# Performance work log

Measured on AMD Instinct MI355X. Metric: run time of the kernel, lower is better.

The kernel has to match this reference:

```python
import jax, jax.numpy as jnp
import numpy as np

N_HEAD = 8  # config.n_head

def _ln(x, g, b):
    # eqx.nn.LayerNorm, eps=1e-5
    m = x.mean(-1, keepdims=True)
    v = ((x - m) ** 2).mean(-1, keepdims=True)
    return (x - m) / jnp.sqrt(v + 1e-5) * g + b

def _lin(x, w, b):
    # eqx.nn.Linear: weight [out, in]
    return x @ w.T + b

def _heads(t):
    B, T, C = t.shape
    return t.reshape(B, T, N_HEAD, C // N_HEAD).transpose(0, 2, 1, 3)  # [B,H,T,d]

def _merge(t):
    B, H, T, d = t.shape
    return t.transpose(0, 2, 1, 3).reshape(B, T, H * d)

def setup_inputs() -> dict:
    key = jax.random.key(0)
    B, T1, T2, C, INNER, NIN = 4, 4096, 4096, 512, 2048, 2
    ks = jax.random.split(key, 16)
    w = lambda k, *s: 0.02 * jax.random.normal(k, s, dtype=jnp.float32)
    return {
        'x': jax.random.normal(ks[0], (B, T1, C), dtype=jnp.float32),
        'ys': jax.random.normal(ks[1], (NIN, B, T2, C), dtype=jnp.float32),
        'ln1_g': jnp.ones((C,)), 'ln1_b': jnp.zeros((C,)),
        'ln2_g': jnp.ones((NIN, C)), 'ln2_b': jnp.zeros((NIN, C)),
        'ln3_g': jnp.ones((C,)), 'ln3_b': jnp.zeros((C,)),
        'ln4_g': jnp.ones((C,)), 'ln4_b': jnp.zeros((C,)),
        'ln5_g': jnp.ones((C,)), 'ln5_b': jnp.zeros((C,)),
        'ca_wq': w(ks[2], C, C), 'ca_bq': jnp.zeros((C,)),
        'ca_wk': w(ks[3], NIN, C, C), 'ca_bk': jnp.zeros((NIN, C)),
        'ca_wv': w(ks[4], NIN, C, C), 'ca_bv': jnp.zeros((NIN, C)),
        'ca_wo': w(ks[5], C, C), 'ca_bo': jnp.zeros((C,)),
        'sa_wq': w(ks[6], C, C), 'sa_bq': jnp.zeros((C,)),
        'sa_wk': w(ks[7], C, C), 'sa_bk': jnp.zeros((C,)),
        'sa_wv': w(ks[8], C, C), 'sa_bv': jnp.zeros((C,)),
        'sa_wo': w(ks[9], C, C), 'sa_bo': jnp.zeros((C,)),
        'ffn1_w1': w(ks[10], INNER, C), 'ffn1_b1': jnp.zeros((INNER,)),
        'ffn1_w2': w(ks[11], C, INNER), 'ffn1_b2': jnp.zeros((C,)),
        'ffn2_w1': w(ks[12], INNER, C), 'ffn2_b1': jnp.zeros((INNER,)),
        'ffn2_w2': w(ks[13], C, INNER), 'ffn2_b2': jnp.zeros((C,)),
    }

def reference(x, ys, ln1_g, ln1_b, ln2_g, ln2_b, ln3_g, ln3_b, ln4_g, ln4_b, ln5_g, ln5_b,
              ca_wq, ca_bq, ca_wk, ca_bk, ca_wv, ca_bv, ca_wo, ca_bo,
              sa_wq, sa_bq, sa_wk, sa_bk, sa_wv, sa_bv, sa_wo, sa_bo,
              ffn1_w1, ffn1_b1, ffn1_w2, ffn1_b2, ffn2_w1, ffn2_b1, ffn2_w2, ffn2_b2):
    n_inputs = ys.shape[0]
    # ---- linear cross attention ----
    xn = _ln(x, ln1_g, ln1_b)
    q = jax.nn.softmax(_heads(_lin(xn, ca_wq, ca_bq)), axis=-1)  # [B,H,T1,d]
    out = q
    for i in range(n_inputs):  # small fixed branch count
        yn = _ln(ys[i], ln2_g[i], ln2_b[i])
        k = jax.nn.softmax(_heads(_lin(yn, ca_wk[i], ca_bk[i])), axis=-1)  # [B,H,T2,d]
        v = _heads(_lin(yn, ca_wv[i], ca_bv[i]))
        k_sum = k.sum(axis=-2, keepdims=True)                       # [B,H,1,d]
        D_inv = 1.0 / ((q * k_sum).sum(axis=-1, keepdims=True) + 1e-8)
        ctx = jnp.einsum('bhnd,bhnv->bhdv', k, v)                   # [B,H,d,d]
        out = out + jnp.einsum('bhqd,bhdv->bhqv', q, ctx) * D_inv
    x = x + _lin(_merge(out), ca_wo, ca_bo)
    # ---- FFN 1 ----
    xn = _ln(x, ln3_g, ln3_b)
    x = x + _lin(jax.nn.gelu(_lin(xn, ffn1_w1, ffn1_b1)), ffn1_w2, ffn1_b2)
    # ---- linear self attention (attn_type='l1') ----
    xn = _ln(x, ln4_g, ln4_b)
    q = jax.nn.softmax(_heads(_lin(xn, sa_wq, sa_bq)), axis=-1)
    k = jax.nn.softmax(_heads(_lin(xn, sa_wk, sa_bk)), axis=-1)
    v = _heads(_lin(xn, sa_wv, sa_bv))
    k_sum = k.sum(axis=-2, keepdims=True)
    D_inv = 1.0 / (q * k_sum).sum(axis=-1, keepdims=True)  # no eps in 'l1' branch
    ctx = jnp.einsum('bhnd,bhnv->bhdv', k, v)
    sa = jnp.einsum('bhqd,bhdv->bhqv', q, ctx) * D_inv + q
    x = x + _lin(_merge(sa), sa_wo, sa_bo)
    # ---- FFN 2 ----
    xn = _ln(x, ln5_g, ln5_b)
    x = x + _lin(jax.nn.gelu(_lin(xn, ffn2_w1, ffn2_b1)), ffn2_w2, ffn2_b2)
    return x
```

## Files before the change

kernel.cpp:

```cpp
#include <hip/hip_runtime.h>
#include <hip/hip_bf16.h>
#include <math.h>
#include <stdint.h>

typedef unsigned short u16;
typedef __attribute__((ext_vector_type(8))) short bh8;
typedef __attribute__((ext_vector_type(4))) float fx4;

#define DEV static __device__ __forceinline__

DEV float bf2f(u16 u){ union{unsigned u; float f;} v; v.u = ((unsigned)u)<<16; return v.f; }
DEV u16 f2bf(float f){ union{float f; unsigned u;} v; v.f = f;
  return (u16)((v.u + 0x7fffu + ((v.u>>16)&1u))>>16); }

DEV void async16(const u16* g, u16* l){
  __builtin_amdgcn_global_load_lds((__attribute__((address_space(1))) void*)(uintptr_t)g,
                                   (__attribute__((address_space(3))) void*)l, 16, 0, 0);
}

DEV size_t faddr(int row, int col, int Kbuf){
  return (size_t)(row>>4)*((size_t)Kbuf*16)
       + (size_t)((col>>3)*128 + (row&15)*8 + (col&7));
}

DEV float gelu_fast(float x){
  float x2 = x*x;
  float t  = __builtin_fmaf(x2, -0.071354816f, -1.5957691216f);
  float e  = __expf(x*t);
  return __fdividef(x, 1.f + e);
}

DEV int2 xcd_swz(){
  const int gx  = gridDim.x;
  const int ord = blockIdx.y*gx + blockIdx.x;
  const int nwg = gx*gridDim.y;
  const int wg  = (ord&7)*(nwg>>3) + (ord>>3);
  int2 r; r.x = wg % gx; r.y = wg / gx; return r;
}

struct WDesc { const float* src[14]; int off[14]; };
__global__ __launch_bounds__(256) void convw_kernel(WDesc d, u16* __restrict__ dst){
  int i = blockIdx.x*256 + threadIdx.x;
  int s = 0;
  #pragma unroll
  for(int j=1;j<14;j++) if(i >= d.off[j]) s = j;
  dst[i] = f2bf(d.src[s][i - d.off[s]]);
}

DEV float wsum64(float s){
  s += __shfl_xor(s,1,64);  s += __shfl_xor(s,2,64);  s += __shfl_xor(s,4,64);
  s += __shfl_xor(s,8,64);  s += __shfl_xor(s,16,64); s += __shfl_xor(s,32,64);
  return s;
}
DEV void ln_row(const float* xrow, const float* g, const float* bta, u16* orow, int lane){
  const float4* xr = (const float4*)xrow + lane*2;
  float4 a = xr[0], c = xr[1];
  float s = a.x+a.y+a.z+a.w + c.x+c.y+c.z+c.w;
  float mean = wsum64(s) * (1.f/512.f);
  float d0=a.x-mean,d1=a.y-mean,d2=a.z-mean,d3=a.w-mean;
  float d4=c.x-mean,d5=c.y-mean,d6=c.z-mean,d7=c.w-mean;
  float sv = d0*d0+d1*d1+d2*d2+d3*d3+d4*d4+d5*d5+d6*d6+d7*d7;
  float rstd = rsqrtf(wsum64(sv)*(1.f/512.f) + 1e-5f);
  const float4* gr = (const float4*)g   + lane*2;
  const float4* br = (const float4*)bta + lane*2;
  float4 g0=gr[0], g1=gr[1], b0=br[0], b1=br[1];
  bh8 o;
  o[0]=(short)f2bf(d0*rstd*g0.x+b0.x); o[1]=(short)f2bf(d1*rstd*g0.y+b0.y);
  o[2]=(short)f2bf(d2*rstd*g0.z+b0.z); o[3]=(short)f2bf(d3*rstd*g0.w+b0.w);
  o[4]=(short)f2bf(d4*rstd*g1.x+b1.x); o[5]=(short)f2bf(d5*rstd*g1.y+b1.y);
  o[6]=(short)f2bf(d6*rstd*g1.z+b1.z); o[7]=(short)f2bf(d7*rstd*g1.w+b1.w);
  *(bh8*)(orow + (size_t)lane*128) = o;
}
__global__ __launch_bounds__(256) void ln_kernel(const float* __restrict__ x,
    const float* __restrict__ g, const float* __restrict__ bta, u16* __restrict__ out){
  int row  = blockIdx.x*4 + (threadIdx.x>>6);
  u16* orow = out + (size_t)(row>>4)*8192 + (size_t)(row&15)*8;
  ln_row(x + (size_t)row*512, g, bta, orow, threadIdx.x&63);
}
__global__ __launch_bounds__(256) void lny_kernel(const float* __restrict__ ys,
    const float* __restrict__ g2, const float* __restrict__ b2, u16* __restrict__ out){
  int row  = blockIdx.x*4 + (threadIdx.x>>6);
  int i = row>>14;
  u16* orow = out + (size_t)(row>>4)*8192 + (size_t)(row&15)*8;
  ln_row(ys + (size_t)row*512, g2 + i*512, b2 + i*512, orow, threadIdx.x&63);
}

#define BSTAGE128(Wb, K, kk, buf)                                                    \
    async16(Wb + (size_t)srow*(K)      + (kk) + scol, &lsB[buf][(w*32   )*32]);      \
    async16(Wb + (size_t)(srow+16)*(K) + (kk) + scol, &lsB[buf][(w*32+16)*32]);

#define APREF4(AF, K, kk)                                                            \
    _Pragma("unroll")                                                                \
    for(int t=0;t<4;t++)                                                             \
      AF[t] = *(const bh8*)(Alane + (size_t)t*16*(K) + (size_t)(kk)*16);

#define MFMA128(AF, CUR)                                                             \
    { bh8 bfx[4];                                                                    \
      _Pragma("unroll")                                                              \
      for(int t=0;t<4;t++)                                                           \
        bfx[t] = *(const bh8*)&lsB[CUR][(wn*64+t*16+l15)*32 + rsw*8];                \
      _Pragma("unroll")                                                              \
      for(int mt=0;mt<4;mt++)                                                        \
        _Pragma("unroll")                                                            \
        for(int nt=0;nt<4;nt++)                                                      \
          acc[mt][nt] = __builtin_amdgcn_mfma_f32_16x16x32_bf16(AF[mt], bfx[nt], acc[mt][nt], 0,0,0); }

#define CSTEP128(AFU, AFP, CUR, jj, Wb, K)                                           \
    if((jj)+1<NS){                                                                   \
      BSTAGE128(Wb, K, ((jj)+1)*32, (CUR)^1)                                         \
      asm volatile("" ::: "memory");                                                 \
      APREF4(AFP, K, ((jj)+1)*32)                                                    \
      asm volatile("s_waitcnt vmcnt(10)" ::: "memory");                              \
    } else {                                                                         \
      asm volatile("s_waitcnt vmcnt(0)" ::: "memory");                               \
    }                                                                                \
    __builtin_amdgcn_s_barrier();                                                    \
    MFMA128(AFU, CUR)                                                                \
    __builtin_amdgcn_s_barrier();

#define KLOOP_CNT128(Ab, Wb, K, WTILE)                                               \
  const int srow = w*32 + (lane>>2);                                                 \
  const int scol = (((lane&3) ^ ((srow>>1)&3)) * 8);                                 \
  const int rsw  = ((l15>>1)&3) ^ quad;                                              \
  const u16* Alane = (Ab) + (size_t)(WTILE)*16*(K) + lane*8;                         \
  bh8 afA[4], afB[4];                                                                \
  BSTAGE128(Wb, K, 0, 0)                                                             \
  asm volatile("" ::: "memory");                                                     \
  APREF4(afA, K, 0)                                                                  \
  const int NS = (K)>>5;                                                             \
  for(int j=0;j<NS;j+=2){                                                            \
    CSTEP128(afA, afB, 0, j,   Wb, K)                                                \
    CSTEP128(afB, afA, 1, j+1, Wb, K)                                                \
  }

#define SSTEP128(AFU, AFP, CUR, jj, Wb, K)                                           \
    if((jj)+1<NS){                                                                   \
      BSTAGE128(Wb, K, ((jj)+1)*32, (CUR)^1)                                         \
      APREF4(AFP, K, ((jj)+1)*32)                                                    \
    }                                                                                \
    MFMA128(AFU, CUR)                                                                \
    __syncthreads();

#define KLOOP_SYNC128(Ab, Wb, K, WTILE)                                              \
  const int srow = w*32 + (lane>>2);                                                 \
  const int scol = (((lane&3) ^ ((srow>>1)&3)) * 8);                                 \
  const int rsw  = ((l15>>1)&3) ^ quad;                                              \
  const u16* Alane = (Ab) + (size_t)(WTILE)*16*(K) + lane*8;                         \
  bh8 afA[4], afB[4];                                                                \
  BSTAGE128(Wb, K, 0, 0)                                                             \
  APREF4(afA, K, 0)                                                                  \
  __syncthreads();                                                                   \
  const int NS = (K)>>5;                                                             \
  for(int j=0;j<NS;j+=2){                                                            \
    SSTEP128(afA, afB, 0, j,   Wb, K)                                                \
    SSTEP128(afB, afA, 1, j+1, Wb, K)                                                \
  }

#define BSTAGE64(Wb, K, kk, buf)                                                     \
    async16(Wb + (size_t)browB*(K) + (kk) + scolB, &lsB[buf][(w*16)*32]);

#define APREF2(AF, K, kk)                                                            \
    _Pragma("unroll")                                                                \
    for(int t=0;t<2;t++)                                                             \
      AF[t] = *(const bh8*)(Alane + (size_t)t*16*(K) + (size_t)(kk)*16);

#define MFMA64(AF, CUR)                                                              \
    { bh8 bfx[4];                                                                    \
      _Pragma("unroll")                                                              \
      for(int t=0;t<4;t++)                                                           \
        bfx[t] = *(const bh8*)&lsB[CUR][(t*16+l15)*32 + rsw*8];                      \
      _Pragma("unroll")                                                              \
      for(int mt=0;mt<2;mt++)                                                        \
        _Pragma("unroll")                                                            \
        for(int nt=0;nt<4;nt++)                                                      \
          acc[mt][nt] = __builtin_amdgcn_mfma_f32_16x16x32_bf16(AF[mt], bfx[nt], acc[mt][nt], 0,0,0); }

#define CSTEP64(AFU, AFP, CUR, jj, Wb, K)                                            \
    if((jj)+1<NS){                                                                   \
      BSTAGE64(Wb, K, ((jj)+1)*32, (CUR)^1)                                          \
      asm volatile("" ::: "memory");                                                 \
      APREF2(AFP, K, ((jj)+1)*32)                                                    \
      asm volatile("s_waitcnt vmcnt(5)" ::: "memory");                               \
    } else {                                                                         \
      asm volatile("s_waitcnt vmcnt(0)" ::: "memory");                               \
    }                                                                                \
    __builtin_amdgcn_s_barrier();                                                    \
    MFMA64(AFU, CUR)                                                                 \
    __builtin_amdgcn_s_barrier();

#define KLOOP_CNT64(Ab, Wb, K)                                                       \
  const int browB = w*16 + (lane>>2);                                                \
  const int scolB = (((lane&3) ^ ((browB>>1)&3)) * 8);                               \
  const int rsw   = ((l15>>1)&3) ^ quad;                                             \
  const u16* Alane = (Ab) + (size_t)(w*2)*16*(K) + lane*8;                           \
  bh8 afA[2], afB[2];                                                                \
  BSTAGE64(Wb, K, 0, 0)                                                              \
  asm volatile("" ::: "memory");                                                     \
  APREF2(afA, K, 0)                                                                  \
  const int NS = (K)>>5;                                                             \
  for(int j=0;j<NS;j+=2){                                                            \
    CSTEP64(afA, afB, 0, j,   Wb, K)                                                 \
    CSTEP64(afB, afA, 1, j+1, Wb, K)                                                 \
  }

struct SubD { const float* bias; u16* out; float* ksum; int mode; };
struct Subs3 { SubD s[3]; };
__global__ __launch_bounds__(256) void gemm_qkv(const u16* __restrict__ A,
    const u16* __restrict__ W, Subs3 subs, int K, int wstride, int bstride, int ksstride){
  __shared__ __align__(16) u16 lsB[2][128*32];
  const int tid = threadIdx.x, lane = tid&63, w = tid>>6;
  const int quad = lane>>4, l15 = lane&15;
  const int2 swz = xcd_swz();
  const int bn = swz.x, bm = swz.y;
  const int iset = bm>>7;
  const int wm = w&1, wn = w>>1;
  fx4 acc[4][4];
  #pragma unroll
  for(int i=0;i<4;i++)
    #pragma unroll
    for(int j=0;j<4;j++) acc[i][j] = (fx4){0.f,0.f,0.f,0.f};
  const u16* Ab = A + (size_t)bm*128*K;
  const u16* Wb = W + (size_t)iset*wstride + (size_t)bn*128*K;
  KLOOP_CNT128(Ab, Wb, K, wm*4)
  const SubD sub = subs.s[bn>>2];
  const int colw = (bn&3)*128 + wn*64;
  const float* bias = sub.bias + iset*bstride;
  float bcol[4];
  #pragma unroll
  for(int nt=0;nt<4;nt++) bcol[nt] = bias[colw + nt*16 + l15];

  if(sub.mode==1){
    float ksacc[4] = {0.f,0.f,0.f,0.f};
    #pragma unroll
    for(int mt=0;mt<4;mt++)
      #pragma unroll
      for(int r=0;r<4;r++){
        float v0=acc[mt][0][r]+bcol[0], v1=acc[mt][1][r]+bcol[1];
        float v2=acc[mt][2][r]+bcol[2], v3=acc[mt][3][r]+bcol[3];
        float mx = fmaxf(fmaxf(v0,v1),fmaxf(v2,v3));
        mx = fmaxf(mx,__shfl_xor(mx,1,64)); mx = fmaxf(mx,__shfl_xor(mx,2,64));
        mx = fmaxf(mx,__shfl_xor(mx,4,64)); mx = fmaxf(mx,__shfl_xor(mx,8,64));
        float e0=__expf(v0-mx), e1=__expf(v1-mx), e2=__expf(v2-mx), e3=__expf(v3-mx);
        float s = e0+e1+e2+e3;
        s += __shfl_xor(s,1,64); s += __shfl_xor(s,2,64);
        s += __shfl_xor(s,4,64); s += __shfl_xor(s,8,64);
        float inv = __fdividef(1.f, s);
        e0*=inv; e1*=inv; e2*=inv; e3*=inv;
        ksacc[0]+=e0; ksacc[1]+=e1; ksacc[2]+=e2; ksacc[3]+=e3;
        int row = bm*128 + wm*64 + mt*16 + quad*4 + r;
        size_t rb = (size_t)row*512;
        sub.out[rb+colw+ 0+l15]=f2bf(e0); sub.out[rb+colw+16+l15]=f2bf(e1);
        sub.out[rb+colw+32+l15]=f2bf(e2); sub.out[rb+colw+48+l15]=f2bf(e3);
      }
    if(sub.ksum){
      int b = (bm&127)>>5;
      float* ks = sub.ksum + iset*ksstride + b*512;
      #pragma unroll
      for(int nt=0;nt<4;nt++){
        float s = ksacc[nt];
        s += __shfl_xor(s,16,64); s += __shfl_xor(s,32,64);
        if(quad==0) atomicAdd(&ks[colw + nt*16 + l15], s);
      }
    }
  } else {
    #pragma unroll
    for(int mt=0;mt<4;mt++)
      #pragma unroll
      for(int r=0;r<4;r++){
        int row = bm*128 + wm*64 + mt*16 + quad*4 + r;
        size_t rb = (size_t)row*512;
        #pragma unroll
        for(int nt=0;nt<4;nt++)
          sub.out[rb + colw + nt*16 + l15] = f2bf(acc[mt][nt][r] + bcol[nt]);
      }
  }
}

__global__ __launch_bounds__(256) void gemm_q64(const u16* __restrict__ A,
    const u16* __restrict__ W, const float* __restrict__ bias, u16* __restrict__ out){
  __shared__ __align__(16) u16 lsB[2][64*32];
  const int tid = threadIdx.x, lane = tid&63, w = tid>>6;
  const int quad = lane>>4, l15 = lane&15;
  const int2 swz = xcd_swz();
  const int bn = swz.x, bm = swz.y;
  fx4 acc[2][4];
  #pragma unroll
  for(int i=0;i<2;i++)
    #pragma unroll
    for(int j=0;j<4;j++) acc[i][j] = (fx4){0.f,0.f,0.f,0.f};
  const u16* Ab = A + (size_t)bm*128*512;
  const u16* Wb = W + (size_t)bn*64*512;
  KLOOP_CNT64(Ab, Wb, 512)
  const int colb = bn*64;
  float bcol[4];
  #pragma unroll
  for(int nt=0;nt<4;nt++) bcol[nt] = bias[colb + nt*16 + l15];
  #pragma unroll
  for(int mt=0;mt<2;mt++)
    #pragma unroll
    for(int r=0;r<4;r++){
      float v0=acc[mt][0][r]+bcol[0], v1=acc[mt][1][r]+bcol[1];
      float v2=acc[mt][2][r]+bcol[2], v3=acc[mt][3][r]+bcol[3];
      float mx = fmaxf(fmaxf(v0,v1),fmaxf(v2,v3));
      mx = fmaxf(mx,__shfl_xor(mx,1,64)); mx = fmaxf(mx,__shfl_xor(mx,2,64));
      mx = fmaxf(mx,__shfl_xor(mx,4,64)); mx = fmaxf(mx,__shfl_xor(mx,8,64));
      float e0=__expf(v0-mx), e1=__expf(v1-mx), e2=__expf(v2-mx), e3=__expf(v3-mx);
      float s = e0+e1+e2+e3;
      s += __shfl_xor(s,1,64); s += __shfl_xor(s,2,64);
      s += __shfl_xor(s,4,64); s += __shfl_xor(s,8,64);
      float inv = __fdividef(1.f, s);
      e0*=inv; e1*=inv; e2*=inv; e3*=inv;
      int row = bm*128 + w*32 + mt*16 + quad*4 + r;
      size_t rb = (size_t)row*512;
      out[rb+colb+ 0+l15]=f2bf(e0); out[rb+colb+16+l15]=f2bf(e1);
      out[rb+colb+32+l15]=f2bf(e2); out[rb+colb+48+l15]=f2bf(e3);
    }
}

__global__ __launch_bounds__(256) void gemm_dn64(const u16* __restrict__ A,
    const u16* __restrict__ W, const float* __restrict__ bias,
    const float* __restrict__ res, float* __restrict__ out, int N, int K){
  __shared__ __align__(16) u16 lsB[2][64*32];
  const int tid = threadIdx.x, lane = tid&63, w = tid>>6;
  const int quad = lane>>4, l15 = lane&15;
  const int2 swz = xcd_swz();
  const int bn = swz.x, bm = swz.y;
  fx4 acc[2][4];
  #pragma unroll
  for(int i=0;i<2;i++)
    #pragma unroll
    for(int j=0;j<4;j++) acc[i][j] = (fx4){0.f,0.f,0.f,0.f};
  const u16* Ab = A + (size_t)bm*128*K;
  const u16* Wb = W + (size_t)bn*64*K;
  KLOOP_CNT64(Ab, Wb, K)
  const int colb = bn*64;
  float bcol[4];
  #pragma unroll
  for(int nt=0;nt<4;nt++) bcol[nt] = bias[colb + nt*16 + l15];
  #pragma unroll
  for(int mt=0;mt<2;mt++)
    #pragma unroll
    for(int r=0;r<4;r++){
      int row = bm*128 + w*32 + mt*16 + quad*4 + r;
      size_t rb = (size_t)row*N;
      #pragma unroll
      for(int nt=0;nt<4;nt++){
        int col = colb + nt*16 + l15;
        out[rb+col] = res[rb+col] + acc[mt][nt][r] + bcol[nt];
      }
    }
}

__global__ __launch_bounds__(256) void gemm_up(const u16* __restrict__ A,
    const u16* __restrict__ W, const float* __restrict__ bias,
    u16* __restrict__ out, int N, int K){
  __shared__ __align__(16) u16 lsB[2][128*32];
  const int tid = threadIdx.x, lane = tid&63, w = tid>>6;
  const int quad = lane>>4, l15 = lane&15;
  const int2 swz = xcd_swz();
  const int bn = swz.x, bm = swz.y;
  const int wm = w&1, wn = w>>1;
  fx4 acc[4][4];
  #pragma unroll
  for(int i=0;i<4;i++)
    #pragma unroll
    for(int j=0;j<4;j++) acc[i][j] = (fx4){0.f,0.f,0.f,0.f};
  const u16* Ab = A + (size_t)bm*128*K;
  const u16* Wb = W + (size_t)bn*128*K;
  KLOOP_SYNC128(Ab, Wb, K, wm*4)
  const int colbase = bn*128 + wn*64;
  float bcol[4];
  #pragma unroll
  for(int nt=0;nt<4;nt++) bcol[nt] = bias[colbase + nt*16 + l15];
  #pragma unroll
  for(int mt=0;mt<4;mt++)
    #pragma unroll
    for(int r=0;r<4;r++){
      int row = bm*128 + wm*64 + mt*16 + quad*4 + r;
      #pragma unroll
      for(int nt=0;nt<4;nt++){
        int col = colbase + nt*16 + l15;
        out[faddr(row, col, N)] = f2bf(gelu_fast(acc[mt][nt][r] + bcol[nt]));
      }
    }
}

__global__ __launch_bounds__(256) void ctx_kernel(const u16* __restrict__ kb,
    const u16* __restrict__ vb, float* __restrict__ ctx, size_t kstride){
  __shared__ __align__(16) u16 lk[64*72];
  __shared__ __align__(16) u16 lv[64*72];
  const int tid=threadIdx.x, lane=tid&63, w=tid>>6, quad=lane>>4, l15=lane&15;
  const int bh2 = blockIdx.x, i = bh2>>5, h = bh2&7, b = (bh2>>3)&3;
  const u16* kbase = kb + (size_t)i*kstride;
  const u16* vbase = vb + (size_t)i*kstride;
  const size_t rowbase = (size_t)b*4096 + (size_t)blockIdx.y*512;
  const int mt0=(w&1)*32, nt0=(w>>1)*32;
  fx4 acc[2][2];
  #pragma unroll
  for(int x=0;x<2;x++)
    #pragma unroll
    for(int j=0;j<2;j++) acc[x][j] = (fx4){0.f,0.f,0.f,0.f};
  const int tl = tid>>2, part = tid&3;
  for(int it=0; it<8; it++){
    __syncthreads();
    {
      size_t gro = (rowbase + it*64 + tl)*512 + h*64 + part*16;
      bh8 k0 = *(const bh8*)(kbase + gro); bh8 k1 = *(const bh8*)(kbase + gro + 8);
      bh8 v0 = *(const bh8*)(vbase + gro); bh8 v1 = *(const bh8*)(vbase + gro + 8);
      #pragma unroll
      for(int j=0;j<8;j++){
        lk[(part*16+j  )*72 + tl] = (u16)k0[j];
        lk[(part*16+8+j)*72 + tl] = (u16)k1[j];
        lv[(part*16+j  )*72 + tl] = (u16)v0[j];
        lv[(part*16+8+j)*72 + tl] = (u16)v1[j];
      }
    }
    __syncthreads();
    #pragma unroll
    for(int ks=0;ks<2;ks++){
      bh8 a0 = *(const bh8*)&lk[(mt0    +l15)*72 + ks*32 + quad*8];
      bh8 a1 = *(const bh8*)&lk[(mt0+16 +l15)*72 + ks*32 + quad*8];
      bh8 b0 = *(const bh8*)&lv[(nt0    +l15)*72 + ks*32 + quad*8];
      bh8 b1 = *(const bh8*)&lv[(nt0+16 +l15)*72 + ks*32 + quad*8];
      acc[0][0] = __builtin_amdgcn_mfma_f32_16x16x32_bf16(a0,b0,acc[0][0],0,0,0);
      acc[0][1] = __builtin_amdgcn_mfma_f32_16x16x32_bf16(a0,b1,acc[0][1],0,0,0);
      acc[1][0] = __builtin_amdgcn_mfma_f32_16x16x32_bf16(a1,b0,acc[1][0],0,0,0);
      acc[1][1] = __builtin_amdgcn_mfma_f32_16x16x32_bf16(a1,b1,acc[1][1],0,0,0);
    }
  }
  float* cb = ctx + (size_t)bh2*4096;
  #pragma unroll
  for(int mi=0;mi<2;mi++)
    #pragma unroll
    for(int ni=0;ni<2;ni++)
      #pragma unroll
      for(int r=0;r<4;r++){
        int d1 = mt0 + mi*16 + quad*4 + r;
        int d2 = nt0 + ni*16 + l15;
        atomicAdd(&cb[d1*64 + d2], acc[mi][ni][r]);
      }
}

template<int NIN>
__global__ __launch_bounds__(256) void apply_kernel(const u16* __restrict__ q,
    const float* __restrict__ ctx, const float* __restrict__ ksum, float eps,
    u16* __restrict__ out){
  __shared__ __align__(16) u16 lctx[(NIN+1)*64*72];
  const int tid=threadIdx.x, lane=tid&63, w=tid>>6, quad=lane>>4, l15=lane&15;
  const int bh = blockIdx.x, b=bh>>3, h=bh&7;
  {
    int base = tid*16;
    int d1 = base>>6, d2b = base&63;
    #pragma unroll
    for(int s=0;s<=NIN;s++){
      u16* dst = &lctx[s*64*72];
      if(s<NIN){
        const float* sp = ctx + ((size_t)s*32 + bh)*4096 + base;
        #pragma unroll
        for(int j=0;j<16;j++) dst[(d2b+j)*72 + d1] = f2bf(sp[j]);
      } else {
        #pragma unroll
        for(int j=0;j<16;j++) dst[(d2b+j)*72 + d1] = ((d2b+j)==d1) ? (u16)0x3f80 : (u16)0;
      }
    }
  }
  float kslo[NIN][8], kshi[NIN][8];
  #pragma unroll
  for(int s=0;s<NIN;s++){
    const float* ks = ksum + s*2048 + b*512 + h*64;
    #pragma unroll
    for(int j=0;j<8;j++){ kslo[s][j] = ks[quad*8+j]; kshi[s][j] = ks[32+quad*8+j]; }
  }
  __syncthreads();
  bh8 bfr[NIN+1][4][2];
  #pragma unroll
  for(int s=0;s<=NIN;s++)
    #pragma unroll
    for(int nt=0;nt<4;nt++)
      #pragma unroll
      for(int ks=0;ks<2;ks++)
        bfr[s][nt][ks] = *(const bh8*)&lctx[s*64*72 + (nt*16+l15)*72 + ks*32 + quad*8];
  const size_t tb0 = (size_t)b*4096 + (size_t)blockIdx.y*256 + w*64;
  for(int g=0;g<4;g++){
    size_t tb = tb0 + g*16;
    const u16* qr = q + (tb + l15)*512 + h*64;
    bh8 a0 = *(const bh8*)(qr + quad*8);
    bh8 a1 = *(const bh8*)(qr + 32 + quad*8);
    float dv[NIN][4];
    #pragma unroll
    for(int s=0;s<NIN;s++){
      float part = 0.f;
      #pragma unroll
      for(int j=0;j<8;j++)
        part += bf2f((u16)a0[j])*kslo[s][j] + bf2f((u16)a1[j])*kshi[s][j];
      part += __shfl_xor(part,16,64); part += __shfl_xor(part,32,64);
      #pragma unroll
      for(int r=0;r<4;r++)
        dv[s][r] = __fdividef(1.f, __shfl(part, quad*4+r, 64) + eps);
    }
    fx4 outv[4];
    #pragma unroll
    for(int nt=0;nt<4;nt++) outv[nt] = (fx4){0.f,0.f,0.f,0.f};
    #pragma unroll
    for(int s=0;s<=NIN;s++){
      fx4 c[4];
      #pragma unroll
      for(int nt=0;nt<4;nt++){
        c[nt] = (fx4){0.f,0.f,0.f,0.f};
        c[nt] = __builtin_amdgcn_mfma_f32_16x16x32_bf16(a0, bfr[s][nt][0], c[nt], 0,0,0);
        c[nt] = __builtin_amdgcn_mfma_f32_16x16x32_bf16(a1, bfr[s][nt][1], c[nt], 0,0,0);
      }
      #pragma unroll
      for(int nt=0;nt<4;nt++)
        #pragma unroll
        for(int r=0;r<4;r++) outv[nt][r] += c[nt][r]*((s==NIN)?1.f:dv[s][r]);
    }
    #pragma unroll
    for(int nt=0;nt<4;nt++)
      #pragma unroll
      for(int r=0;r<4;r++)
        out[faddr((int)tb + quad*4 + r, h*64 + nt*16 + l15, 512)] = f2bf(outv[nt][r]);
  }
}

extern "C" void kernel_launch(void* const* d_in, const int* in_sizes, int n_in,
                              void* d_out, int out_size, void* d_ws, size_t ws_size,
                              hipStream_t stream){
  const float* x_in =(const float*)d_in[0];
  const float* ys   =(const float*)d_in[1];
  const float* ln1g =(const float*)d_in[2],  *ln1b=(const float*)d_in[3];
  const float* ln2g =(const float*)d_in[4],  *ln2b=(const float*)d_in[5];
  const float* ln3g =(const float*)d_in[6],  *ln3b=(const float*)d_in[7];
  const float* ln4g =(const float*)d_in[8],  *ln4b=(const float*)d_in[9];
  const float* ln5g =(const float*)d_in[10], *ln5b=(const float*)d_in[11];
  const float* ca_wq=(const float*)d_in[12], *ca_bq=(const float*)d_in[13];
  const float* ca_wk=(const float*)d_in[14], *ca_bk=(const float*)d_in[15];
  const float* ca_wv=(const float*)d_in[16], *ca_bv=(const float*)d_in[17];
  const float* ca_wo=(const float*)d_in[18], *ca_bo=(const float*)d_in[19];
  const float* sa_wq=(const float*)d_in[20], *sa_bq=(const float*)d_in[21];
  const float* sa_wk=(const float*)d_in[22], *sa_bk=(const float*)d_in[23];
  const float* sa_wv=(const float*)d_in[24], *sa_bv=(const float*)d_in[25];
  const float* sa_wo=(const float*)d_in[26], *sa_bo=(const float*)d_in[27];
  const float* f1w1 =(const float*)d_in[28], *f1b1=(const float*)d_in[29];
  const float* f1w2 =(const float*)d_in[30], *f1b2=(const float*)d_in[31];
  const float* f2w1 =(const float*)d_in[32], *f2b1=(const float*)d_in[33];
  const float* f2w2 =(const float*)d_in[34], *f2b2=(const float*)d_in[35];

  char* p = (char*)d_ws;
  u16*   WBF = (u16*)p;    p += 13631488;
  float* XW  = (float*)p;  p += 33554432;
  u16*   XN2 = (u16*)p;    p += 33554432;
  u16*   QB  = (u16*)p;    p += 16777216;
  u16*   R1  = (u16*)p;    p += 67108864;
  u16*   OUTB= (u16*)p;    p += 16777216;
  float* SM  = (float*)p;  p += 1597440;
  u16*   XN  = XN2;
  u16*   KB2 = R1;
  u16*   VB2 = R1 + 16777216;
  u16*   HB  = R1;
  float* CTXC = SM;
  float* CTXS = SM + 262144;
  float* KSC  = SM + 393216;
  float* KSS  = SM + 397312;

  WDesc wd;
  const float* wsrc[14] = {ca_wq, ca_wk, ca_wv, ca_wk+262144, ca_wv+262144, ca_wo,
                           sa_wq, sa_wk, sa_wv, sa_wo, f1w1, f1w2, f2w1, f2w2};
  const int    woff[14] = {0, 262144, 524288, 786432, 1048576, 1310720,
                           1572864, 1835008, 2097152, 2359296,
                           2621440, 3670016, 4718592, 5767168};
  for(int i=0;i<14;i++){ wd.src[i]=wsrc[i]; wd.off[i]=woff[i]; }
  convw_kernel<<<26624,256,0,stream>>>(wd, WBF);
  hipMemsetAsync(SM, 0, 399360*sizeof(float), stream);

  SubD zsub = {nullptr,nullptr,nullptr,0};

  ln_kernel<<<4096,256,0,stream>>>(x_in, ln1g, ln1b, OUTB);
  lny_kernel<<<8192,256,0,stream>>>(ys, ln2g, ln2b, XN2);
  gemm_q64<<<dim3(8,128),256,0,stream>>>(OUTB, WBF+0, ca_bq, QB);
  { Subs3 s = {{ {ca_bk, KB2, KSC, 1}, {ca_bv, VB2, nullptr, 0}, zsub }};
    gemm_qkv<<<dim3(8,256),256,0,stream>>>(XN2, WBF+262144, s, 512,
                                           524288, 512, 2048); }
  ctx_kernel<<<dim3(64,8),256,0,stream>>>(KB2, VB2, CTXC, (size_t)16384*512);
  apply_kernel<2><<<dim3(32,16),256,0,stream>>>(QB, CTXC, KSC, 1e-8f, OUTB);
  gemm_dn64<<<dim3(8,128),256,0,stream>>>(OUTB, WBF+1310720, ca_bo, x_in, XW, 512, 512);

  ln_kernel<<<4096,256,0,stream>>>(XW, ln3g, ln3b, XN);
  gemm_up<<<dim3(16,128),256,0,stream>>>(XN, WBF+2621440, f1b1, HB, 2048, 512);
  gemm_dn64<<<dim3(8,128),256,0,stream>>>(HB, WBF+3670016, f1b2, XW, XW, 512, 2048);

  ln_kernel<<<4096,256,0,stream>>>(XW, ln4g, ln4b, XN);
  { Subs3 s = {{ {sa_bq, QB, nullptr, 1}, {sa_bk, KB2, KSS, 1}, {sa_bv, VB2, nullptr, 0} }};
    gemm_qkv<<<dim3(12,128),256,0,stream>>>(XN, WBF+1572864, s, 512, 0,0,0); }
  ctx_kernel<<<dim3(32,8),256,0,stream>>>(KB2, VB2, CTXS, 0);
  apply_kernel<1><<<dim3(32,16),256,0,stream>>>(QB, CTXS, KSS, 0.f, OUTB);
  gemm_dn64<<<dim3(8,128),256,0,stream>>>(OUTB, WBF+2359296, sa_bo, XW, XW, 512, 512);

  ln_kernel<<<4096,256,0,stream>>>(XW, ln5g, ln5b, XN);
  gemm_up<<<dim3(16,128),256,0,stream>>>(XN, WBF+4718592, f2b1, HB, 2048, 512);
  gemm_dn64<<<dim3(8,128),256,0,stream>>>(HB, WBF+5767168, f2b2, XW, (float*)d_out, 512, 2048);
}
```

Before: 692.5 us.

## Deepen A-fragment register prefetch to two steps ahead in GEMM K-loops

Restructures the counted K-loops so the A-operand register fragments are prefetched two K-steps ahead, issued right after the MFMA block, instead of one step ahead alongside the B staging. The vmcnt waits are loosened accordingly so only the B tile for the current step must have landed. It also precomputes per-lane base pointers for the global A and B addresses to cut address arithmetic. The aim is to hide global load latency for A behind more MFMA work, at the cost of fragile hand-tuned waitcnt values and extra live registers.

New measurement: 745.1 us. +7.6%, slower.

```diff
diff --git a/kernel.cpp b/kernel.cpp
--- a/kernel.cpp
+++ b/kernel.cpp
@@ -8,6 +8,7 @@
 typedef __attribute__((ext_vector_type(4))) float fx4;
 
 #define DEV static __device__ __forceinline__
+#define PIN asm volatile("" ::: "memory");
 
 DEV float bf2f(u16 u){ union{unsigned u; float f;} v; v.u = ((unsigned)u)<<16; return v.f; }
 DEV u16 f2bf(float f){ union{float f; unsigned u;} v; v.f = f;
@@ -85,14 +86,14 @@
   ln_row(ys + (size_t)row*512, g2 + i*512, b2 + i*512, orow, threadIdx.x&63);
 }
 
-#define BSTAGE128(Wb, K, kk, buf)                                                    \
-    async16(Wb + (size_t)srow*(K)      + (kk) + scol, &lsB[buf][(w*32   )*32]);      \
-    async16(Wb + (size_t)(srow+16)*(K) + (kk) + scol, &lsB[buf][(w*32+16)*32]);
-
-#define APREF4(AF, K, kk)                                                            \
+#define PREF4s(F, step)                                                              \
     _Pragma("unroll")                                                                \
     for(int t=0;t<4;t++)                                                             \
-      AF[t] = *(const bh8*)(Alane + (size_t)t*16*(K) + (size_t)(kk)*16);
+      F[t] = *(const bh8*)(Ap + (size_t)t*AS + (size_t)(step)*512);
+#define PREF2s(F, step)                                                              \
+    _Pragma("unroll")                                                                \
+    for(int t=0;t<2;t++)                                                             \
+      F[t] = *(const bh8*)(Ap + (size_t)t*AS + (size_t)(step)*512);
 
 #define MFMA128(AF, CUR)                                                             \
     { bh8 bfx[4];                                                                    \
@@ -105,65 +106,6 @@
         for(int nt=0;nt<4;nt++)                                                      \
           acc[mt][nt] = __builtin_amdgcn_mfma_f32_16x16x32_bf16(AF[mt], bfx[nt], acc[mt][nt], 0,0,0); }
 
-#define CSTEP128(AFU, AFP, CUR, jj, Wb, K)                                           \
-    if((jj)+1<NS){                                                                   \
-      BSTAGE128(Wb, K, ((jj)+1)*32, (CUR)^1)                                         \
-      asm volatile("" ::: "memory");                                                 \
-      APREF4(AFP, K, ((jj)+1)*32)                                                    \
-      asm volatile("s_waitcnt vmcnt(10)" ::: "memory");                              \
-    } else {                                                                         \
-      asm volatile("s_waitcnt vmcnt(0)" ::: "memory");                               \
-    }                                                                                \
-    __builtin_amdgcn_s_barrier();                                                    \
-    MFMA128(AFU, CUR)                                                                \
-    __builtin_amdgcn_s_barrier();
-
-#define KLOOP_CNT128(Ab, Wb, K, WTILE)                                               \
-  const int srow = w*32 + (lane>>2);                                                 \
-  const int scol = (((lane&3) ^ ((srow>>1)&3)) * 8);                                 \
-  const int rsw  = ((l15>>1)&3) ^ quad;                                              \
-  const u16* Alane = (Ab) + (size_t)(WTILE)*16*(K) + lane*8;                         \
-  bh8 afA[4], afB[4];                                                                \
-  BSTAGE128(Wb, K, 0, 0)                                                             \
-  asm volatile("" ::: "memory");                                                     \
-  APREF4(afA, K, 0)                                                                  \
-  const int NS = (K)>>5;                                                             \
-  for(int j=0;j<NS;j+=2){                                                            \
-    CSTEP128(afA, afB, 0, j,   Wb, K)                                                \
-    CSTEP128(afB, afA, 1, j+1, Wb, K)                                                \
-  }
-
-#define SSTEP128(AFU, AFP, CUR, jj, Wb, K)                                           \
-    if((jj)+1<NS){                                                                   \
-      BSTAGE128(Wb, K, ((jj)+1)*32, (CUR)^1)                                         \
-      APREF4(AFP, K, ((jj)+1)*32)                                                    \
-    }                                                                                \
-    MFMA128(AFU, CUR)                                                                \
-    __syncthreads();
-
-#define KLOOP_SYNC128(Ab, Wb, K, WTILE)                                              \
-  const int srow = w*32 + (lane>>2);                                                 \
-  const int scol = (((lane&3) ^ ((srow>>1)&3)) * 8);                                 \
-  const int rsw  = ((l15>>1)&3) ^ quad;                                              \
-  const u16* Alane = (Ab) + (size_t)(WTILE)*16*(K) + lane*8;                         \
-  bh8 afA[4], afB[4];                                                                \
-  BSTAGE128(Wb, K, 0, 0)                                                             \
-  APREF4(afA, K, 0)                                                                  \
-  __syncthreads();                                                                   \
-  const int NS = (K)>>5;                                                             \
-  for(int j=0;j<NS;j+=2){                                                            \
-    SSTEP128(afA, afB, 0, j,   Wb, K)                                                \
-    SSTEP128(afB, afA, 1, j+1, Wb, K)                                                \
-  }
-
-#define BSTAGE64(Wb, K, kk, buf)                                                     \
-    async16(Wb + (size_t)browB*(K) + (kk) + scolB, &lsB[buf][(w*16)*32]);
-
-#define APREF2(AF, K, kk)                                                            \
-    _Pragma("unroll")                                                                \
-    for(int t=0;t<2;t++)                                                             \
-      AF[t] = *(const bh8*)(Alane + (size_t)t*16*(K) + (size_t)(kk)*16);
-
 #define MFMA64(AF, CUR)                                                              \
     { bh8 bfx[4];                                                                    \
       _Pragma("unroll")                                                              \
@@ -175,32 +117,110 @@
         for(int nt=0;nt<4;nt++)                                                      \
           acc[mt][nt] = __builtin_amdgcn_mfma_f32_16x16x32_bf16(AF[mt], bfx[nt], acc[mt][nt], 0,0,0); }
 
-#define CSTEP64(AFU, AFP, CUR, jj, Wb, K)                                            \
-    if((jj)+1<NS){                                                                   \
-      BSTAGE64(Wb, K, ((jj)+1)*32, (CUR)^1)                                          \
-      asm volatile("" ::: "memory");                                                 \
-      APREF2(AFP, K, ((jj)+1)*32)                                                    \
-      asm volatile("s_waitcnt vmcnt(5)" ::: "memory");                               \
-    } else {                                                                         \
-      asm volatile("s_waitcnt vmcnt(0)" ::: "memory");                               \
+#define KLOOP_CNT128(Ab, Wb, K, WTILE)                                               \
+  const int srow = w*32 + (lane>>2);                                                 \
+  const int scol = (((lane&3) ^ ((srow>>1)&3)) * 8);                                 \
+  const int rsw  = ((l15>>1)&3) ^ quad;                                              \
+  const u16* Bg0 = (Wb) + (size_t)srow*(K) + scol;                                   \
+  const u16* Bg1 = (Wb) + (size_t)(srow+16)*(K) + scol;                              \
+  const u16* Ap  = (Ab) + (size_t)(WTILE)*16*(K) + lane*8;                           \
+  const size_t AS = (size_t)16*(K);                                                  \
+  bh8 afA[4], afB[4];                                                                \
+  async16(Bg0, &lsB[0][(w*32)*32]); async16(Bg1, &lsB[0][(w*32+16)*32]);             \
+  PIN                                                                                \
+  PREF4s(afA, 0)                                                                     \
+  PIN                                                                                \
+  PREF4s(afB, 1)                                                                     \
+  PIN                                                                                \
+  const int NS = (K)>>5;                                                             \
+  for(int j=0;j<NS;j+=2){                                                            \
+    if(j+1<NS){ async16(Bg0+(j+1)*32, &lsB[1][(w*32)*32]);                           \
+                async16(Bg1+(j+1)*32, &lsB[1][(w*32+16)*32]);                        \
+                PIN                                                                  \
+                asm volatile("s_waitcnt vmcnt(6)" ::: "memory"); }                   \
+    else      { asm volatile("s_waitcnt vmcnt(0)" ::: "memory"); }                   \
+    __builtin_amdgcn_s_barrier();                                                    \
+    MFMA128(afA, 0)                                                                  \
+    if(j+2<NS){ PREF4s(afA, j+2) PIN }                                               \
+    __builtin_amdgcn_s_barrier();                                                    \
+    if(j+1<NS){                                                                      \
+      if(j+2<NS){ async16(Bg0+(j+2)*32, &lsB[0][(w*32)*32]);                         \
+                  async16(Bg1+(j+2)*32, &lsB[0][(w*32+16)*32]);                      \
+                  PIN                                                                \
+                  asm volatile("s_waitcnt vmcnt(6)" ::: "memory"); }                 \
+      else      { asm volatile("s_waitcnt vmcnt(0)" ::: "memory"); }                 \
+      __builtin_amdgcn_s_barrier();                                                  \
+      MFMA128(afB, 1)                                                                \
+      if(j+3<NS){ PREF4s(afB, j+3) PIN }                                             \
+      __builtin_amdgcn_s_barrier();                                                  \
     }                                                                                \
-    __builtin_amdgcn_s_barrier();                                                    \
-    MFMA64(AFU, CUR)                                                                 \
-    __builtin_amdgcn_s_barrier();
+  }
+
+#define KLOOP_SYNC128(Ab, Wb, K, WTILE)                                              \
+  const int srow = w*32 + (lane>>2);                                                 \
+  const int scol = (((lane&3) ^ ((srow>>1)&3)) * 8);                                 \
+  const int rsw  = ((l15>>1)&3) ^ quad;                                              \
+  const u16* Bg0 = (Wb) + (size_t)srow*(K) + scol;                                   \
+  const u16* Bg1 = (Wb) + (size_t)(srow+16)*(K) + scol;                              \
+  const u16* Ap  = (Ab) + (size_t)(WTILE)*16*(K) + lane*8;                           \
+  const size_t AS = (size_t)16*(K);                                                  \
+  bh8 afA[4], afB[4];                                                                \
+  async16(Bg0, &lsB[0][(w*32)*32]); async16(Bg1, &lsB[0][(w*32+16)*32]);             \
+  PIN                                                                                \
+  PREF4s(afA, 0)                                                                     \
+  __syncthreads();                                                                   \
+  const int NS = (K)>>5;                                                             \
+  for(int j=0;j<NS;j+=2){                                                            \
+    if(j+1<NS){ async16(Bg0+(j+1)*32, &lsB[1][(w*32)*32]);                           \
+                async16(Bg1+(j+1)*32, &lsB[1][(w*32+16)*32]);                        \
+                PIN                                                                  \
+                PREF4s(afB, j+1) }                                                   \
+    MFMA128(afA, 0)                                                                  \
+    __syncthreads();                                                                 \
+    if(j+1<NS){                                                                      \
+      if(j+2<NS){ async16(Bg0+(j+2)*32, &lsB[0][(w*32)*32]);                         \
+                  async16(Bg1+(j+2)*32, &lsB[0][(w*32+16)*32]);                      \
+                  PIN                                                                \
+                  PREF4s(afA, j+2) }                                                 \
+      MFMA128(afB, 1)                                                                \
+      __syncthreads();                                                               \
+    }                                                                                \
+  }
 
 #define KLOOP_CNT64(Ab, Wb, K)                                                       \
   const int browB = w*16 + (lane>>2);                                                \
   const int scolB = (((lane&3) ^ ((browB>>1)&3)) * 8);                               \
   const int rsw   = ((l15>>1)&3) ^ quad;                                             \
-  const u16* Alane = (Ab) + (size_t)(w*2)*16*(K) + lane*8;                           \
+  const u16* Bg = (Wb) + (size_t)browB*(K) + scolB;                                  \
+  const u16* Ap = (Ab) + (size_t)(w*2)*16*(K) + lane*8;                              \
+  const size_t AS = (size_t)16*(K);                                                  \
   bh8 afA[2], afB[2];                                                                \
-  BSTAGE64(Wb, K, 0, 0)                                                              \
-  asm volatile("" ::: "memory");                                                     \
-  APREF2(afA, K, 0)                                                                  \
+  async16(Bg, &lsB[0][(w*16)*32]);                                                   \
+  PIN                                                                                \
+  PREF2s(afA, 0)                                                                     \
+  PIN                                                                                \
+  PREF2s(afB, 1)                                                                     \
+  PIN                                                                                \
   const int NS = (K)>>5;                                                             \
   for(int j=0;j<NS;j+=2){                                                            \
-    CSTEP64(afA, afB, 0, j,   Wb, K)                                                 \
-    CSTEP64(afB, afA, 1, j+1, Wb, K)                                                 \
+    if(j+1<NS){ async16(Bg+(j+1)*32, &lsB[1][(w*16)*32]);                            \
+                PIN                                                                  \
+                asm volatile("s_waitcnt vmcnt(3)" ::: "memory"); }                   \
+    else      { asm volatile("s_waitcnt vmcnt(0)" ::: "memory"); }                   \
+    __builtin_amdgcn_s_barrier();                                                    \
+    MFMA64(afA, 0)                                                                   \
+    if(j+2<NS){ PREF2s(afA, j+2) PIN }                                               \
+    __builtin_amdgcn_s_barrier();                                                    \
+    if(j+1<NS){                                                                      \
+      if(j+2<NS){ async16(Bg+(j+2)*32, &lsB[0][(w*16)*32]);                          \
+                  PIN                                                                \
+                  asm volatile("s_waitcnt vmcnt(3)" ::: "memory"); }                 \
+      else      { asm volatile("s_waitcnt vmcnt(0)" ::: "memory"); }                 \
+      __builtin_amdgcn_s_barrier();                                                  \
+      MFMA64(afB, 1)                                                                 \
+      if(j+3<NS){ PREF2s(afB, j+3) PIN }                                             \
+      __builtin_amdgcn_s_barrier();                                                  \
+    }                                                                                \
   }
 
 struct SubD { const float* bias; u16* out; float* ksum; int mode; };
```
